# Kernel optimization log

Measured on AMD Instinct MI355X. Metric: run time of the kernel, lower is better.

Reference implementation:

```python
import jax, jax.numpy as jnp
import numpy as np
import math

B, L, D, H = 4, 2048, 1024, 16
DK = D // H

def setup_inputs() -> dict:
    key = jax.random.key(0)
    ks = jax.random.split(key, 12)
    inp = {
        'query': jax.random.normal(ks[0], (B, L, D), dtype=jnp.float32),
        'key':   jax.random.normal(ks[1], (B, L, D), dtype=jnp.float32),
        'value': jax.random.normal(ks[2], (B, L, D), dtype=jnp.float32),
        # causal mask, broadcast over batch: [B, L, L], 1 = keep, 0 = masked
        'mask': jnp.broadcast_to(jnp.tril(jnp.ones((L, L), dtype=jnp.int32)), (B, L, L)),
    }
    s = 1.0 / math.sqrt(D)
    inp['Wq'] = jax.random.uniform(ks[3], (D, D), jnp.float32, -s, s)
    inp['bq'] = jax.random.uniform(ks[4], (D,), jnp.float32, -s, s)
    inp['Wk'] = jax.random.uniform(ks[5], (D, D), jnp.float32, -s, s)
    inp['bk'] = jax.random.uniform(ks[6], (D,), jnp.float32, -s, s)
    inp['Wv'] = jax.random.uniform(ks[7], (D, D), jnp.float32, -s, s)
    inp['bv'] = jax.random.uniform(ks[8], (D,), jnp.float32, -s, s)
    inp['Wo'] = jax.random.uniform(ks[9], (D, D), jnp.float32, -s, s)
    inp['bo'] = jax.random.uniform(ks[10], (D,), jnp.float32, -s, s)
    return inp

def reference(query, key, value, mask, Wq, bq, Wk, bk, Wv, bv, Wo, bo):
    # projections (torch Linear: x @ W.T + b), split heads: [B, H, L, DK]
    def proj(x, W, b):
        return (x @ W.T + b).reshape(B, -1, H, DK).transpose(0, 2, 1, 3)
    q = proj(query, Wq, bq)
    k = proj(key, Wk, bk)
    v = proj(value, Wv, bv)
    scores = jnp.einsum('bhqd,bhkd->bhqk', q, k) / math.sqrt(DK)
    scores = jnp.where(mask[:, None, :, :] == 0, jnp.float32(-1e9), scores)
    p_attn = jax.nn.softmax(scores, axis=-1)  # dropout p=0.0 -> identity
    x = jnp.einsum('bhqk,bhkd->bhqd', p_attn, v)
    x = x.transpose(0, 2, 1, 3).reshape(B, -1, D)
    return x @ Wo.T + bo
```

## Files before the change

### kernel.cpp

```cpp
#include <hip/hip_runtime.h>
#include <hip/hip_bf16.h>

#define B_ 4
#define H_ 16
#define L_ 2048
#define D_ 1024
#define DK_ 64

typedef __attribute__((ext_vector_type(8))) __bf16 bf16x8;
typedef __attribute__((ext_vector_type(4))) __bf16 bf16x4;
typedef __attribute__((ext_vector_type(4))) float f32x4;

#define MFMA16(a, b, c) __builtin_amdgcn_mfma_f32_16x16x32_bf16(a, b, c, 0, 0, 0)

typedef const __attribute__((address_space(1))) void gv_t;
typedef __attribute__((address_space(3))) void lv_t;

template<int NI>
__device__ __forceinline__ void stage_swz(const __bf16* __restrict__ g,
                                          size_t gstride, __bf16* lds, int t)
{
    const int wave = t >> 6;
#pragma unroll
    for (int i = 0; i < NI; ++i) {
        const int row = i * 32 + (t >> 3);
        const int s   = (t & 7) ^ (row & 7);
        __builtin_amdgcn_global_load_lds(
            (gv_t*)(g + (size_t)row * gstride + s * 8),
            (lv_t*)(lds + (size_t)(i * 32 + wave * 8) * 64),
            16, 0, 0);
    }
}

__device__ __forceinline__ bf16x8 lds_frag(const __bf16* base, int row, int kbyte)
{
    const char* p = (const char*)base + row * 128 + (kbyte ^ ((row & 7) << 4));
    return *(const bf16x8*)p;
}

struct CastArgs {
    const float* s[7];
    __bf16*      d[7];
    int          n[7];
};

__global__ __launch_bounds__(256)
void cast_all(CastArgs a)
{
    const int seg = blockIdx.y;
    const int n   = a.n[seg];
    const float* __restrict__ s = a.s[seg];
    __bf16* __restrict__ d = a.d[seg];
    for (int i = (blockIdx.x * 256 + threadIdx.x) * 8; i < n; i += gridDim.x * 256 * 8) {
        float4 f0 = *reinterpret_cast<const float4*>(&s[i]);
        float4 f1 = *reinterpret_cast<const float4*>(&s[i + 4]);
        bf16x8 v;
        v[0] = (__bf16)f0.x; v[1] = (__bf16)f0.y; v[2] = (__bf16)f0.z; v[3] = (__bf16)f0.w;
        v[4] = (__bf16)f1.x; v[5] = (__bf16)f1.y; v[6] = (__bf16)f1.z; v[7] = (__bf16)f1.w;
        *reinterpret_cast<bf16x8*>(&d[i]) = v;
    }
}

template<int MODE>
__global__ __launch_bounds__(256)
void gemm_bf16(const __bf16* __restrict__ A, const __bf16* __restrict__ W,
               const float* __restrict__ bias, void* __restrict__ Cout,
               int M, int N, int K)
{
    constexpr int BM = 128, BN = 128, BK = 64;
    __shared__ __bf16 As[2][BM * BK];
    __shared__ __bf16 Bs[2][BN * BK];

    const int t = threadIdx.x;
    const int wave = t >> 6, lane = t & 63;
    const int g4 = lane >> 4, l16 = lane & 15;
    const int wr = wave >> 1, wc = wave & 1;
    const int fid  = blockIdx.x;
    const int fid2 = (fid & 7) * 64 + (fid >> 3);
    const int m0 = (fid2 >> 3) * BM;
    const int n0 = (fid2 & 7) * BN;

    f32x4 acc[4][4];
#pragma unroll
    for (int m = 0; m < 4; ++m)
#pragma unroll
        for (int n = 0; n < 4; ++n) acc[m][n] = {0.f, 0.f, 0.f, 0.f};

    const int nt = K / BK;
    stage_swz<4>(A + (size_t)m0 * K, (size_t)K, As[0], t);
    stage_swz<4>(W + (size_t)n0 * K, (size_t)K, Bs[0], t);
    __syncthreads();

    int cur = 0;
    for (int ti = 0; ti < nt; ++ti) {
        if (ti + 1 < nt) {
            stage_swz<4>(A + (size_t)m0 * K + (ti + 1) * BK, (size_t)K, As[cur ^ 1], t);
            stage_swz<4>(W + (size_t)n0 * K + (ti + 1) * BK, (size_t)K, Bs[cur ^ 1], t);
        }
#pragma unroll
        for (int kk = 0; kk < 2; ++kk) {
            bf16x8 af[4], bfr[4];
#pragma unroll
            for (int m = 0; m < 4; ++m)
                af[m] = lds_frag(As[cur], wr * 64 + m * 16 + l16, kk * 64 + g4 * 16);
#pragma unroll
            for (int n = 0; n < 4; ++n)
                bfr[n] = lds_frag(Bs[cur], wc * 64 + n * 16 + l16, kk * 64 + g4 * 16);
#pragma unroll
            for (int m = 0; m < 4; ++m)
#pragma unroll
                for (int n = 0; n < 4; ++n)
                    acc[m][n] = MFMA16(af[m], bfr[n], acc[m][n]);
        }
        __syncthreads();
        cur ^= 1;
    }

    float bv[4];
#pragma unroll
    for (int n = 0; n < 4; ++n) bv[n] = bias[n0 + wc * 64 + n * 16 + l16];

#pragma unroll
    for (int m = 0; m < 4; ++m) {
#pragma unroll
        for (int n = 0; n < 4; ++n) {
            const int gc = n0 + wc * 64 + n * 16 + l16;
            const int gr0 = m0 + wr * 64 + m * 16 + g4 * 4;
            if (MODE == 0) {
                const int hh = gc >> 6, dk = gc & (DK_ - 1);
#pragma unroll
                for (int r = 0; r < 4; ++r) {
                    const int gr = gr0 + r;
                    const int bb = gr >> 11, l = gr & (L_ - 1);
                    ((__bf16*)Cout)[(((size_t)(bb * H_ + hh)) * L_ + l) * DK_ + dk] =
                        (__bf16)(acc[m][n][r] + bv[n]);
                }
            } else if (MODE == 1) {
                const int hh = gc >> 6, dk = gc & (DK_ - 1);
                const int bb = gr0 >> 11, l0 = gr0 & (L_ - 1);
                bf16x4 v;
#pragma unroll
                for (int r = 0; r < 4; ++r) v[r] = (__bf16)(acc[m][n][r] + bv[n]);
                *reinterpret_cast<bf16x4*>(
                    &((__bf16*)Cout)[(((size_t)(bb * H_ + hh)) * DK_ + dk) * L_ + l0]) = v;
            } else {
#pragma unroll
                for (int r = 0; r < 4; ++r)
                    ((float*)Cout)[(size_t)(gr0 + r) * N + gc] = acc[m][n][r] + bv[n];
            }
        }
    }
}

#define SCALE2 0.18033688011112042f

__global__ __launch_bounds__(256)
void attn_mfma(const __bf16* __restrict__ Qh, const __bf16* __restrict__ Kh,
               const __bf16* __restrict__ Vt, __bf16* __restrict__ Xb)
{
    __shared__ __bf16 Ks[2][64 * 64];
    __shared__ __bf16 Vs[2][64 * 64];
    __shared__ __bf16 Ps[64 * 64];

    const int t = threadIdx.x;
    const int wave = t >> 6, lane = t & 63;
    const int g4 = lane >> 4, l16 = lane & 15;
    const int fid   = blockIdx.x;
    const int xcd   = fid & 7;
    const int idx   = fid >> 3;
    const int strip = 31 - (idx >> 3);
    const int hb_id = xcd * 8 + (idx & 7);
    const int h = hb_id & 15, b = hb_id >> 4;
    const int qb = strip * 64;
    const size_t hb = (size_t)(b * H_ + h) * L_ * DK_;
    const __bf16* Qp = Qh + hb;
    const __bf16* Kp = Kh + hb;
    const __bf16* Vp = Vt + hb;
    const int qrow0 = qb + wave * 16;

    bf16x8 qf[2];
#pragma unroll
    for (int kk = 0; kk < 2; ++kk)
        qf[kk] = *reinterpret_cast<const bf16x8*>(
            &Qp[(size_t)(qrow0 + l16) * DK_ + kk * 32 + g4 * 8]);

    f32x4 O[4];
    float m_run[4], l_run[4];
#pragma unroll
    for (int r = 0; r < 4; ++r) { m_run[r] = -1e30f; l_run[r] = 0.f; }
#pragma unroll
    for (int n = 0; n < 4; ++n) O[n] = {0.f, 0.f, 0.f, 0.f};

    const int ntile = strip + 1;
    stage_swz<2>(Kp, DK_, Ks[0], t);
    stage_swz<2>(Vp, L_, Vs[0], t);
    __syncthreads();

    int cur = 0;
    for (int it = 0; it < ntile; ++it) {
        if (it + 1 < ntile) {
            stage_swz<2>(Kp + (size_t)(it + 1) * 64 * DK_, DK_, Ks[cur ^ 1], t);
            stage_swz<2>(Vp + (it + 1) * 64, L_, Vs[cur ^ 1], t);
        }
        const int kv0 = it * 64;

        f32x4 s[4];
#pragma unroll
        for (int n = 0; n < 4; ++n) s[n] = {0.f, 0.f, 0.f, 0.f};
        __builtin_amdgcn_s_setprio(1);
#pragma unroll
        for (int kk = 0; kk < 2; ++kk) {
            bf16x8 kf[4];
#pragma unroll
            for (int n = 0; n < 4; ++n)
                kf[n] = lds_frag(Ks[cur], n * 16 + l16, kk * 64 + g4 * 16);
#pragma unroll
            for (int n = 0; n < 4; ++n)
                s[n] = MFMA16(qf[kk], kf[n], s[n]);
        }
        __builtin_amdgcn_s_setprio(0);

        if (it == strip) {
#pragma unroll
            for (int n = 0; n < 4; ++n)
#pragma unroll
                for (int r = 0; r < 4; ++r) {
                    const int qg = qrow0 + g4 * 4 + r;
                    const int kg = kv0 + n * 16 + l16;
                    s[n][r] = (kg <= qg) ? s[n][r] * SCALE2 : -1e30f;
                }
        } else {
#pragma unroll
            for (int n = 0; n < 4; ++n)
#pragma unroll
                for (int r = 0; r < 4; ++r)
                    s[n][r] *= SCALE2;
        }

        float al[4];
#pragma unroll
        for (int r = 0; r < 4; ++r) {
            float mx = fmaxf(fmaxf(s[0][r], s[1][r]), fmaxf(s[2][r], s[3][r]));
            mx = fmaxf(mx, __shfl_xor(mx, 1));
            mx = fmaxf(mx, __shfl_xor(mx, 2));
            mx = fmaxf(mx, __shfl_xor(mx, 4));
            mx = fmaxf(mx, __shfl_xor(mx, 8));
            const float mn = fmaxf(m_run[r], mx);
            al[r] = exp2f(m_run[r] - mn);
            m_run[r] = mn;
            float lb = 0.f;
#pragma unroll
            for (int n = 0; n < 4; ++n) {
                const float p = exp2f(s[n][r] - mn);
                s[n][r] = p;
                lb += p;
            }
            lb += __shfl_xor(lb, 1);
            lb += __shfl_xor(lb, 2);
            lb += __shfl_xor(lb, 4);
            lb += __shfl_xor(lb, 8);
            l_run[r] = al[r] * l_run[r] + lb;
        }

        char* Pw = (char*)Ps + wave * 16 * 128;
#pragma unroll
        for (int r = 0; r < 4; ++r) {
            const int R = g4 * 4 + r;
#pragma unroll
            for (int n = 0; n < 4; ++n)
                *(__bf16*)(Pw + R * 128 + ((n * 32 + l16 * 2) ^ ((R & 7) << 4))) =
                    (__bf16)s[n][r];
#pragma unroll
            for (int n = 0; n < 4; ++n) O[n][r] *= al[r];
        }

        const __bf16* Pr = Ps + wave * 16 * 64;
        __builtin_amdgcn_s_setprio(1);
#pragma unroll
        for (int kk = 0; kk < 2; ++kk) {
            bf16x8 pa = lds_frag(Pr, l16, kk * 64 + g4 * 16);
            bf16x8 vf[4];
#pragma unroll
            for (int n = 0; n < 4; ++n)
                vf[n] = lds_frag(Vs[cur], n * 16 + l16, kk * 64 + g4 * 16);
#pragma unroll
            for (int n = 0; n < 4; ++n)
                O[n] = MFMA16(pa, vf[n], O[n]);
        }
        __builtin_amdgcn_s_setprio(0);

        __syncthreads();
        cur ^= 1;
    }

#pragma unroll
    for (int r = 0; r < 4; ++r) {
        const float inv = 1.0f / l_run[r];
        const int qrow = qrow0 + g4 * 4 + r;
#pragma unroll
        for (int n = 0; n < 4; ++n)
            Xb[((size_t)b * L_ + qrow) * D_ + h * DK_ + n * 16 + l16] =
                (__bf16)(O[n][r] * inv);
    }
}

extern "C" void kernel_launch(void* const* d_in, const int* in_sizes, int n_in,
                              void* d_out, int out_size, void* d_ws, size_t ws_size,
                              hipStream_t stream)
{
    (void)in_sizes; (void)n_in; (void)out_size; (void)ws_size;
    const float* query = (const float*)d_in[0];
    const float* key   = (const float*)d_in[1];
    const float* value = (const float*)d_in[2];
    const float* Wq = (const float*)d_in[4];
    const float* bq = (const float*)d_in[5];
    const float* Wk = (const float*)d_in[6];
    const float* bk = (const float*)d_in[7];
    const float* Wv = (const float*)d_in[8];
    const float* bv = (const float*)d_in[9];
    const float* Wo = (const float*)d_in[10];
    const float* bo = (const float*)d_in[11];

    const size_t SZ = (size_t)B_ * L_ * D_;
    const size_t WSZ = (size_t)D_ * D_;
    __bf16* wsb = (__bf16*)d_ws;
    __bf16* qb_ = wsb;
    __bf16* kb_ = wsb + SZ;
    __bf16* vb_ = wsb + 2 * SZ;
    __bf16* Qh  = wsb + 3 * SZ;
    __bf16* Kh  = wsb + 4 * SZ;
    __bf16* Vt  = wsb + 5 * SZ;
    __bf16* Xb  = wsb + 6 * SZ;
    __bf16* Wqb = wsb + 7 * SZ;
    __bf16* Wkb = Wqb + WSZ;
    __bf16* Wvb = Wkb + WSZ;
    __bf16* Wob = Wvb + WSZ;

    CastArgs ca;
    ca.s[0] = query; ca.s[1] = key; ca.s[2] = value;
    ca.s[3] = Wq; ca.s[4] = Wk; ca.s[5] = Wv; ca.s[6] = Wo;
    ca.d[0] = qb_; ca.d[1] = kb_; ca.d[2] = vb_;
    ca.d[3] = Wqb; ca.d[4] = Wkb; ca.d[5] = Wvb; ca.d[6] = Wob;
    ca.n[0] = ca.n[1] = ca.n[2] = (int)SZ;
    ca.n[3] = ca.n[4] = ca.n[5] = ca.n[6] = (int)WSZ;
    cast_all<<<dim3(1024, 7), 256, 0, stream>>>(ca);

    const int M = B_ * L_;
    const int ngemm = (M / 128) * (D_ / 128);
    gemm_bf16<0><<<ngemm, 256, 0, stream>>>(qb_, Wqb, bq, Qh, M, D_, D_);
    gemm_bf16<0><<<ngemm, 256, 0, stream>>>(kb_, Wkb, bk, Kh, M, D_, D_);
    gemm_bf16<1><<<ngemm, 256, 0, stream>>>(vb_, Wvb, bv, Vt, M, D_, D_);
    attn_mfma<<<32 * H_ * B_, 256, 0, stream>>>(Qh, Kh, Vt, Xb);
    gemm_bf16<2><<<ngemm, 256, 0, stream>>>(Xb, Wob, bo, d_out, M, D_, D_);
}
```

Baseline: 401.2 us.

## Fuse QKV GEMMs, shrink GEMM tiles, transpose scores and add lazy softmax rescale

Merges the three projection GEMMs into one launch over a concatenated weight buffer, picking the destination layout per output segment. The GEMM tile shrinks to 128x64 with a single LDS buffer and a 4-blocks-per-SM occupancy hint, which drops the double buffering. Attention computes S^T so each lane owns one query row, removing most cross-lane reductions. It also skips rescaling the running max and output unless the max grows past a threshold, trading some exp2 headroom for fewer multiplies.

Result: faster. 349.6 us (-12.9%).

```diff
diff --git a/kernel.cpp b/kernel.cpp
--- a/kernel.cpp
+++ b/kernel.cpp
@@ -61,100 +61,105 @@
     }
 }
 
+struct QKVDst {
+    const float* bq; const float* bk; const float* bvv;
+    __bf16* qh; __bf16* kh; __bf16* vt;
+};
+
+#define ASEG ((size_t)B_ * L_ * D_)
+
 template<int MODE>
-__global__ __launch_bounds__(256)
+__global__ __launch_bounds__(256, 4)
 void gemm_bf16(const __bf16* __restrict__ A, const __bf16* __restrict__ W,
                const float* __restrict__ bias, void* __restrict__ Cout,
-               int M, int N, int K)
-{
-    constexpr int BM = 128, BN = 128, BK = 64;
-    __shared__ __bf16 As[2][BM * BK];
-    __shared__ __bf16 Bs[2][BN * BK];
+               int M, int N, int K, QKVDst qd)
+{
+    constexpr int BM = 128, BN = 64, BK = 64;
+    __shared__ __bf16 As[BM * BK];
+    __shared__ __bf16 Bs[BN * BK];
 
     const int t = threadIdx.x;
     const int wave = t >> 6, lane = t & 63;
     const int g4 = lane >> 4, l16 = lane & 15;
     const int wr = wave >> 1, wc = wave & 1;
-    const int fid  = blockIdx.x;
-    const int fid2 = (fid & 7) * 64 + (fid >> 3);
-    const int m0 = (fid2 >> 3) * BM;
-    const int n0 = (fid2 & 7) * BN;
-
-    f32x4 acc[4][4];
+    const int fid = blockIdx.x;
+    const int idx = fid >> 3;
+    const int m0 = (((fid & 7) << 3) + (idx & 7)) * BM;
+    const int n0 = (idx >> 3) * BN;
+    const int which = (MODE == 3) ? (n0 >> 10) : 0;
+    if (MODE == 3) A += (size_t)which * ASEG;
+
+    f32x4 acc[4][2];
 #pragma unroll
     for (int m = 0; m < 4; ++m)
 #pragma unroll
-        for (int n = 0; n < 4; ++n) acc[m][n] = {0.f, 0.f, 0.f, 0.f};
-
-    const int nt = K / BK;
-    stage_swz<4>(A + (size_t)m0 * K, (size_t)K, As[0], t);
-    stage_swz<4>(W + (size_t)n0 * K, (size_t)K, Bs[0], t);
-    __syncthreads();
-
-    int cur = 0;
-    for (int ti = 0; ti < nt; ++ti) {
-        if (ti + 1 < nt) {
-            stage_swz<4>(A + (size_t)m0 * K + (ti + 1) * BK, (size_t)K, As[cur ^ 1], t);
-            stage_swz<4>(W + (size_t)n0 * K + (ti + 1) * BK, (size_t)K, Bs[cur ^ 1], t);
-        }
+        for (int n = 0; n < 2; ++n) acc[m][n] = {0.f, 0.f, 0.f, 0.f};
+
+    for (int kt = 0; kt < K; kt += BK) {
+        __syncthreads();
+        stage_swz<4>(A + (size_t)m0 * K + kt, (size_t)K, As, t);
+        stage_swz<2>(W + (size_t)n0 * K + kt, (size_t)K, Bs, t);
+        __syncthreads();
 #pragma unroll
         for (int kk = 0; kk < 2; ++kk) {
-            bf16x8 af[4], bfr[4];
+            bf16x8 af[4], bfr[2];
 #pragma unroll
             for (int m = 0; m < 4; ++m)
-                af[m] = lds_frag(As[cur], wr * 64 + m * 16 + l16, kk * 64 + g4 * 16);
-#pragma unroll
-            for (int n = 0; n < 4; ++n)
-                bfr[n] = lds_frag(Bs[cur], wc * 64 + n * 16 + l16, kk * 64 + g4 * 16);
+                af[m] = lds_frag(As, wr * 64 + m * 16 + l16, kk * 64 + g4 * 16);
+#pragma unroll
+            for (int n = 0; n < 2; ++n)
+                bfr[n] = lds_frag(Bs, wc * 32 + n * 16 + l16, kk * 64 + g4 * 16);
 #pragma unroll
             for (int m = 0; m < 4; ++m)
 #pragma unroll
-                for (int n = 0; n < 4; ++n)
+                for (int n = 0; n < 2; ++n)
                     acc[m][n] = MFMA16(af[m], bfr[n], acc[m][n]);
         }
-        __syncthreads();
-        cur ^= 1;
-    }
-
-    float bv[4];
-#pragma unroll
-    for (int n = 0; n < 4; ++n) bv[n] = bias[n0 + wc * 64 + n * 16 + l16];
-
-#pragma unroll
-    for (int m = 0; m < 4; ++m) {
-#pragma unroll
-        for (int n = 0; n < 4; ++n) {
-            const int gc = n0 + wc * 64 + n * 16 + l16;
+    }
+
+#pragma unroll
+    for (int n = 0; n < 2; ++n) {
+        const int gc = n0 + wc * 32 + n * 16 + l16;
+        float bval;
+        int dd = gc, hh = 0, dk = 0;
+        if (MODE == 3) {
+            dd = gc & 1023; hh = dd >> 6; dk = dd & 63;
+            const float* bp = (which == 0) ? qd.bq : (which == 1) ? qd.bk : qd.bvv;
+            bval = bp[dd];
+        } else {
+            bval = bias[gc];
+        }
+#pragma unroll
+        for (int m = 0; m < 4; ++m) {
             const int gr0 = m0 + wr * 64 + m * 16 + g4 * 4;
-            if (MODE == 0) {
-                const int hh = gc >> 6, dk = gc & (DK_ - 1);
-#pragma unroll
-                for (int r = 0; r < 4; ++r) {
-                    const int gr = gr0 + r;
-                    const int bb = gr >> 11, l = gr & (L_ - 1);
-                    ((__bf16*)Cout)[(((size_t)(bb * H_ + hh)) * L_ + l) * DK_ + dk] =
-                        (__bf16)(acc[m][n][r] + bv[n]);
+            if (MODE == 3) {
+                const int bb = gr0 >> 11, l0 = gr0 & (L_ - 1);
+                if (which < 2) {
+                    __bf16* dst = (which == 0) ? qd.qh : qd.kh;
+#pragma unroll
+                    for (int r = 0; r < 4; ++r)
+                        dst[(((size_t)(bb * H_ + hh)) * L_ + l0 + r) * DK_ + dk] =
+                            (__bf16)(acc[m][n][r] + bval);
+                } else {
+                    bf16x4 v;
+#pragma unroll
+                    for (int r = 0; r < 4; ++r) v[r] = (__bf16)(acc[m][n][r] + bval);
+                    *reinterpret_cast<bf16x4*>(
+                        &qd.vt[(((size_t)(bb * H_ + hh)) * DK_ + dk) * L_ + l0]) = v;
                 }
-            } else if (MODE == 1) {
-                const int hh = gc >> 6, dk = gc & (DK_ - 1);
-                const int bb = gr0 >> 11, l0 = gr0 & (L_ - 1);
-                bf16x4 v;
-#pragma unroll
-                for (int r = 0; r < 4; ++r) v[r] = (__bf16)(acc[m][n][r] + bv[n]);
-                *reinterpret_cast<bf16x4*>(
-                    &((__bf16*)Cout)[(((size_t)(bb * H_ + hh)) * DK_ + dk) * L_ + l0]) = v;
             } else {
 #pragma unroll
                 for (int r = 0; r < 4; ++r)
-                    ((float*)Cout)[(size_t)(gr0 + r) * N + gc] = acc[m][n][r] + bv[n];
+                    ((float*)Cout)[(size_t)(gr0 + r) * N + gc] = acc[m][n][r] + bval;
             }
         }
     }
 }
 
 #define SCALE2 0.18033688011112042f
-
-__global__ __launch_bounds__(256)
+#define THR    6.0f
+
+__global__ __launch_bounds__(256, 4)
 void attn_mfma(const __bf16* __restrict__ Qh, const __bf16* __restrict__ Kh,
                const __bf16* __restrict__ Vt, __bf16* __restrict__ Xb)
 {
@@ -185,11 +190,9 @@
             &Qp[(size_t)(qrow0 + l16) * DK_ + kk * 32 + g4 * 8]);
 
     f32x4 O[4];
-    float m_run[4], l_run[4];
-#pragma unroll
-    for (int r = 0; r < 4; ++r) { m_run[r] = -1e30f; l_run[r] = 0.f; }
 #pragma unroll
     for (int n = 0; n < 4; ++n) O[n] = {0.f, 0.f, 0.f, 0.f};
+    float m_run = -1e30f, l_run = 0.f;
 
     const int ntile = strip + 1;
     stage_swz<2>(Kp, DK_, Ks[0], t);
@@ -204,9 +207,9 @@
         }
         const int kv0 = it * 64;
 
-        f32x4 s[4];
-#pragma unroll
-        for (int n = 0; n < 4; ++n) s[n] = {0.f, 0.f, 0.f, 0.f};
+        f32x4 st[4];
+#pragma unroll
+        for (int n = 0; n < 4; ++n) st[n] = {0.f, 0.f, 0.f, 0.f};
         __builtin_amdgcn_s_setprio(1);
 #pragma unroll
         for (int kk = 0; kk < 2; ++kk) {
@@ -216,62 +219,61 @@
                 kf[n] = lds_frag(Ks[cur], n * 16 + l16, kk * 64 + g4 * 16);
 #pragma unroll
             for (int n = 0; n < 4; ++n)
-                s[n] = MFMA16(qf[kk], kf[n], s[n]);
+                st[n] = MFMA16(kf[n], qf[kk], st[n]);
         }
         __builtin_amdgcn_s_setprio(0);
 
         if (it == strip) {
-#pragma unroll
-            for (int n = 0; n < 4; ++n)
-#pragma unroll
-                for (int r = 0; r < 4; ++r) {
-                    const int qg = qrow0 + g4 * 4 + r;
-                    const int kg = kv0 + n * 16 + l16;
-                    s[n][r] = (kg <= qg) ? s[n][r] * SCALE2 : -1e30f;
-                }
-        } else {
+            const int qg = qrow0 + l16;
 #pragma unroll
             for (int n = 0; n < 4; ++n)
 #pragma unroll
                 for (int r = 0; r < 4; ++r)
-                    s[n][r] *= SCALE2;
-        }
-
-        float al[4];
-#pragma unroll
-        for (int r = 0; r < 4; ++r) {
-            float mx = fmaxf(fmaxf(s[0][r], s[1][r]), fmaxf(s[2][r], s[3][r]));
-            mx = fmaxf(mx, __shfl_xor(mx, 1));
-            mx = fmaxf(mx, __shfl_xor(mx, 2));
-            mx = fmaxf(mx, __shfl_xor(mx, 4));
-            mx = fmaxf(mx, __shfl_xor(mx, 8));
-            const float mn = fmaxf(m_run[r], mx);
-            al[r] = exp2f(m_run[r] - mn);
-            m_run[r] = mn;
-            float lb = 0.f;
-#pragma unroll
-            for (int n = 0; n < 4; ++n) {
-                const float p = exp2f(s[n][r] - mn);
-                s[n][r] = p;
+                    if (kv0 + n * 16 + g4 * 4 + r > qg) st[n][r] = -1e30f;
+        }
+
+        float mx = st[0][0];
+#pragma unroll
+        for (int n = 0; n < 4; ++n)
+#pragma unroll
+            for (int r = 0; r < 4; ++r)
+                if (n + r) mx = fmaxf(mx, st[n][r]);
+        mx = fmaxf(mx, __shfl_xor(mx, 16));
+        mx = fmaxf(mx, __shfl_xor(mx, 32));
+        const float mxs = mx * SCALE2;
+
+        const bool grow = !__all(mxs - m_run <= THR);
+        float al = 1.f;
+        if (grow) {
+            const float mn = fmaxf(m_run, mxs);
+            al = exp2f(m_run - mn);
+            m_run = mn;
+        }
+
+        char* Pw = (char*)Ps + (wave * 16 + l16) * 128;
+        float lb = 0.f;
+#pragma unroll
+        for (int n = 0; n < 4; ++n) {
+            bf16x4 pv;
+#pragma unroll
+            for (int r = 0; r < 4; ++r) {
+                const float p = exp2f(fmaf(st[n][r], SCALE2, -m_run));
                 lb += p;
+                pv[r] = (__bf16)p;
             }
-            lb += __shfl_xor(lb, 1);
-            lb += __shfl_xor(lb, 2);
-            lb += __shfl_xor(lb, 4);
-            lb += __shfl_xor(lb, 8);
-            l_run[r] = al[r] * l_run[r] + lb;
-        }
-
-        char* Pw = (char*)Ps + wave * 16 * 128;
-#pragma unroll
-        for (int r = 0; r < 4; ++r) {
-            const int R = g4 * 4 + r;
-#pragma unroll
-            for (int n = 0; n < 4; ++n)
-                *(__bf16*)(Pw + R * 128 + ((n * 32 + l16 * 2) ^ ((R & 7) << 4))) =
-                    (__bf16)s[n][r];
-#pragma unroll
-            for (int n = 0; n < 4; ++n) O[n][r] *= al[r];
+            *(bf16x4*)(Pw + ((n * 32 + g4 * 8) ^ ((l16 & 7) << 4))) = pv;
+        }
+        lb += __shfl_xor(lb, 16);
+        lb += __shfl_xor(lb, 32);
+        l_run = al * l_run + lb;
+
+        if (grow) {
+#pragma unroll
+            for (int r = 0; r < 4; ++r) {
+                const float alr = __shfl(al, g4 * 4 + r);
+#pragma unroll
+                for (int n = 0; n < 4; ++n) O[n][r] *= alr;
+            }
         }
 
         const __bf16* Pr = Ps + wave * 16 * 64;
@@ -293,9 +295,10 @@
         cur ^= 1;
     }
 
+    const float rl = 1.0f / l_run;
 #pragma unroll
     for (int r = 0; r < 4; ++r) {
-        const float inv = 1.0f / l_run[r];
+        const float inv = __shfl(rl, g4 * 4 + r);
         const int qrow = qrow0 + g4 * 4 + r;
 #pragma unroll
         for (int n = 0; n < 4; ++n)
@@ -325,31 +328,29 @@
     const size_t WSZ = (size_t)D_ * D_;
     __bf16* wsb = (__bf16*)d_ws;
     __bf16* qb_ = wsb;
-    __bf16* kb_ = wsb + SZ;
-    __bf16* vb_ = wsb + 2 * SZ;
     __bf16* Qh  = wsb + 3 * SZ;
     __bf16* Kh  = wsb + 4 * SZ;
     __bf16* Vt  = wsb + 5 * SZ;
     __bf16* Xb  = wsb + 6 * SZ;
-    __bf16* Wqb = wsb + 7 * SZ;
-    __bf16* Wkb = Wqb + WSZ;
-    __bf16* Wvb = Wkb + WSZ;
-    __bf16* Wob = Wvb + WSZ;
+    __bf16* Wqkv = wsb + 7 * SZ;
+    __bf16* Wob  = Wqkv + 3 * WSZ;
 
     CastArgs ca;
     ca.s[0] = query; ca.s[1] = key; ca.s[2] = value;
     ca.s[3] = Wq; ca.s[4] = Wk; ca.s[5] = Wv; ca.s[6] = Wo;
-    ca.d[0] = qb_; ca.d[1] = kb_; ca.d[2] = vb_;
-    ca.d[3] = Wqb; ca.d[4] = Wkb; ca.d[5] = Wvb; ca.d[6] = Wob;
+    ca.d[0] = qb_; ca.d[1] = qb_ + SZ; ca.d[2] = qb_ + 2 * SZ;
+    ca.d[3] = Wqkv; ca.d[4] = Wqkv + WSZ; ca.d[5] = Wqkv + 2 * WSZ; ca.d[6] = Wob;
     ca.n[0] = ca.n[1] = ca.n[2] = (int)SZ;
     ca.n[3] = ca.n[4] = ca.n[5] = ca.n[6] = (int)WSZ;
     cast_all<<<dim3(1024, 7), 256, 0, stream>>>(ca);
 
+    QKVDst qd;
+    qd.bq = bq; qd.bk = bk; qd.bvv = bv;
+    qd.qh = Qh; qd.kh = Kh; qd.vt = Vt;
+
     const int M = B_ * L_;
-    const int ngemm = (M / 128) * (D_ / 128);
-    gemm_bf16<0><<<ngemm, 256, 0, stream>>>(qb_, Wqb, bq, Qh, M, D_, D_);
-    gemm_bf16<0><<<ngemm, 256, 0, stream>>>(kb_, Wkb, bk, Kh, M, D_, D_);
-    gemm_bf16<1><<<ngemm, 256, 0, stream>>>(vb_, Wvb, bv, Vt, M, D_, D_);
+    gemm_bf16<3><<<64 * 48, 256, 0, stream>>>(qb_, Wqkv, nullptr, nullptr,
+                                              M, 3 * D_, D_, qd);
     attn_mfma<<<32 * H_ * B_, 256, 0, stream>>>(Qh, Kh, Vt, Xb);
-    gemm_bf16<2><<<ngemm, 256, 0, stream>>>(Xb, Wob, bo, d_out, M, D_, D_);
-}
+    gemm_bf16<2><<<64 * 16, 256, 0, stream>>>(Xb, Wob, bo, d_out, M, D_, D_, qd);
+}
```
